# Kernel tuning notes

Measured on AMD Instinct MI355X. Metric: run time of the kernel, lower is better.

The kernel has to match this reference:

```python
import jax, jax.numpy as jnp
import numpy as np

N = 50000      # nodes
E = 800000     # edges (before self loops)
H = 2          # attention heads
CH = 64        # per-head hidden channels
IN = 128       # input features
OUT = 64       # output channels
EPS = 1e-5     # batchnorm eps
SLOPE = 0.2    # LeakyReLU negative slope


def _gat_conv(x, src, dst, W, a_src, a_dst, b, concat):
    # x: [N, Fin]; W: [Fin, H*C]; a_src/a_dst: [H, C]
    n = x.shape[0]
    h = (x @ W).reshape(n, H, -1)                       # [N, H, C]
    al_s = (h * a_src).sum(-1)                          # [N, H]
    al_d = (h * a_dst).sum(-1)                          # [N, H]
    e = al_s[src] + al_d[dst]                           # [E, H]
    e = jnp.where(e > 0, e, SLOPE * e)                  # LeakyReLU
    # softmax over edges grouped by destination node
    m = jax.ops.segment_max(e, dst, num_segments=n)
    ex = jnp.exp(e - m[dst])
    den = jax.ops.segment_sum(ex, dst, num_segments=n)
    alpha = ex / (den[dst] + 1e-16)                     # [E, H]
    out = jax.ops.segment_sum(h[src] * alpha[:, :, None], dst, num_segments=n)
    out = out.reshape(n, -1) if concat else out.mean(axis=1)
    return out + b


def _batchnorm(x, g, be):
    mu = x.mean(axis=0)
    var = x.var(axis=0)  # biased, as torch BN uses in training
    return (x - mu) * jax.lax.rsqrt(var + EPS) * g + be


def setup_inputs() -> dict:
    key = jax.random.key(0)
    ks = jax.random.split(key, 18)
    s = 0.1
    inp = {
        "x": jax.random.normal(ks[0], (N, IN), jnp.float32),
        "edge_index": jax.random.randint(ks[1], (2, E), 0, N, jnp.int64),
        # layer 0: IN -> H*CH (concat)
        "W0": jax.random.normal(ks[2], (IN, H * CH), jnp.float32) * s,
        "a_src0": jax.random.normal(ks[3], (H, CH), jnp.float32) * s,
        "a_dst0": jax.random.normal(ks[4], (H, CH), jnp.float32) * s,
        "b0": jnp.zeros((H * CH,), jnp.float32),
        "g0": jnp.ones((H * CH,), jnp.float32),
        "be0": jnp.zeros((H * CH,), jnp.float32),
        # layer 1: H*CH -> H*CH (concat)
        "W1": jax.random.normal(ks[5], (H * CH, H * CH), jnp.float32) * s,
        "a_src1": jax.random.normal(ks[6], (H, CH), jnp.float32) * s,
        "a_dst1": jax.random.normal(ks[7], (H, CH), jnp.float32) * s,
        "b1": jnp.zeros((H * CH,), jnp.float32),
        "g1": jnp.ones((H * CH,), jnp.float32),
        "be1": jnp.zeros((H * CH,), jnp.float32),
        # layer 2: H*CH -> OUT, concat=False (mean over heads)
        "W2": jax.random.normal(ks[8], (H * CH, H * OUT), jnp.float32) * s,
        "a_src2": jax.random.normal(ks[9], (H, OUT), jnp.float32) * s,
        "a_dst2": jax.random.normal(ks[10], (H, OUT), jnp.float32) * s,
        "b2": jnp.zeros((OUT,), jnp.float32),
    }
    return inp


def reference(x, edge_index, W0, a_src0, a_dst0, b0, g0, be0,
              W1, a_src1, a_dst1, b1, g1, be1,
              W2, a_src2, a_dst2, b2):
    # add self loops (PyG GATConv default)
    loop = jnp.arange(N, dtype=edge_index.dtype)
    src = jnp.concatenate([edge_index[0], loop])
    dst = jnp.concatenate([edge_index[1], loop])

    h = _gat_conv(x, src, dst, W0, a_src0, a_dst0, b0, concat=True)
    h = jax.nn.relu(_batchnorm(h, g0, be0))
    # dropout: eval mode (identity)
    h = _gat_conv(h, src, dst, W1, a_src1, a_dst1, b1, concat=True)
    h = jax.nn.relu(_batchnorm(h, g1, be1))
    out = _gat_conv(h, src, dst, W2, a_src2, a_dst2, b2, concat=False)
    return out
```

## Files before the change

### kernel.cpp

```cpp
#include <hip/hip_runtime.h>


#define N_NODES 50000
#define N_EDGES 800000
#define ET (N_EDGES + N_NODES)
#define FDIM 128
#define SLOPE 0.2f
#define BN_EPS 1e-5f
#define SCAN_NB 196
#define LOG2E 1.44269504088896340736f
#define WSTRIDE 18432

typedef __attribute__((ext_vector_type(8))) short bf16x8;
typedef __attribute__((ext_vector_type(4))) float f32x4;
typedef __attribute__((ext_vector_type(8))) unsigned short u16x8;

__device__ __forceinline__ unsigned short f2bf(float f) {
  unsigned u = __float_as_uint(f);
  u = u + 0x7fffu + ((u >> 16) & 1u);
  return (unsigned short)(u >> 16);
}
__device__ __forceinline__ float bflo(unsigned p) { return __uint_as_float(p << 16); }
__device__ __forceinline__ float bfhi(unsigned p) { return __uint_as_float(p & 0xffff0000u); }


__global__ __launch_bounds__(256) void hist_rank(const int* __restrict__ dst,
                                                 int* __restrict__ counts,
                                                 int* __restrict__ rank) {
  int i = blockIdx.x * 256 + threadIdx.x;
  if (i >= ET) return;
  int d = (i < N_EDGES) ? dst[i] : i - N_EDGES;
  rank[i] = atomicAdd(&counts[d], 1);
}

__global__ __launch_bounds__(256) void scan_blk(const int* __restrict__ counts,
                                                int* __restrict__ rowptr,
                                                int* __restrict__ partials) {
  int i = blockIdx.x * 256 + threadIdx.x;
  int lane = threadIdx.x & 63, wv = threadIdx.x >> 6;
  int c = (i < N_NODES) ? counts[i] : 0;
  int v = c;
#pragma unroll
  for (int off = 1; off < 64; off <<= 1) {
    int u = __shfl_up(v, off);
    if (lane >= off) v += u;
  }
  __shared__ int wsum[4];
  if (lane == 63) wsum[wv] = v;
  __syncthreads();
  int add = 0;
  for (int w = 0; w < wv; ++w) add += wsum[w];
  if (i < N_NODES) rowptr[i] = v - c + add;
  if (threadIdx.x == 255) partials[blockIdx.x] = add + v;
}

__global__ __launch_bounds__(256) void scan_fin(int* __restrict__ rowptr,
                                                const int* __restrict__ partials) {
  __shared__ int sh[256];
  int t = threadIdx.x;
  sh[t] = (t < (int)blockIdx.x && t < SCAN_NB) ? partials[t] : 0;
  __syncthreads();
#pragma unroll
  for (int off = 128; off > 0; off >>= 1) {
    if (t < off) sh[t] += sh[t + off];
    __syncthreads();
  }
  int base = sh[0];
  int i = blockIdx.x * 256 + t;
  if (i < N_NODES) rowptr[i] += base;
  if (i == 0) rowptr[N_NODES] = ET;
}

__global__ __launch_bounds__(256) void scatter_pos(const int* __restrict__ src,
                                                   const int* __restrict__ dst,
                                                   const int* __restrict__ rowptr,
                                                   const int* __restrict__ rank,
                                                   int* __restrict__ csr_src) {
  int i = blockIdx.x * 256 + threadIdx.x;
  if (i >= ET) return;
  int d, s;
  if (i < N_EDGES) { d = dst[i]; s = src[i]; } else { d = s = i - N_EDGES; }
  csr_src[rowptr[d] + rank[i]] = s;
}

__global__ __launch_bounds__(256) void repack_w(const float* __restrict__ W0,
                                                const float* __restrict__ W1,
                                                const float* __restrict__ W2,
                                                const float* __restrict__ as0,
                                                const float* __restrict__ as1,
                                                const float* __restrict__ as2,
                                                const float* __restrict__ ad0,
                                                const float* __restrict__ ad1,
                                                const float* __restrict__ ad2,
                                                unsigned short* __restrict__ Wr) {
  int i = blockIdx.x * 256 + threadIdx.x;
  if (i >= 3 * WSTRIDE) return;
  int L = i / WSTRIDE, rem = i % WSTRIDE;
  int t  = rem >> 11;
  int ks = (rem >> 9) & 3;
  int ln = (rem >> 3) & 63;
  int j  = rem & 7;
  int k  = ks * 32 + (ln >> 4) * 8 + j;
  const float* W = (L == 0) ? W0 : ((L == 1) ? W1 : W2);
  float val;
  if (t < 8) {
    int col = t * 16 + (ln & 15);
    val = W[k * 128 + col];
  } else {
    int cl = ln & 15;
    if (cl < 4) {
      int head = cl & 1;
      const float* a = (cl < 2) ? ((L == 0) ? as0 : (L == 1) ? as1 : as2)
                                : ((L == 0) ? ad0 : (L == 1) ? ad1 : ad2);
      float s = 0.f;
      const float* wrow = W + k * 128 + head * 64;
      const float* ah = a + head * 64;
#pragma unroll 8
      for (int c = 0; c < 64; ++c) s = fmaf(wrow[c], ah[c], s);
      val = s * LOG2E;
    } else {
      val = 0.f;
    }
  }
  Wr[i] = f2bf(val);
}

__global__ __launch_bounds__(128) void bn_fin(const float* __restrict__ part,
                                              const float* __restrict__ g,
                                              const float* __restrict__ be,
                                              float* __restrict__ lsbuf) {
  int t = threadIdx.x;
  float s = 0.f, q = 0.f;
#pragma unroll
  for (int k = 0; k < 32; ++k) {
    s += part[k * 256 + t];
    q += part[k * 256 + 128 + t];
  }
  float mu  = s * (1.f / N_NODES);
  float var = q * (1.f / N_NODES) - mu * mu;
  float sc  = rsqrtf(var + BN_EPS) * g[t];
  lsbuf[t]       = sc;
  lsbuf[128 + t] = be[t] - mu * sc;
}

__global__ __launch_bounds__(256) void gemm_mfma(const void* __restrict__ Xin,
                                                 const unsigned short* __restrict__ WrL,
                                                 const float* __restrict__ lsbuf,
                                                 unsigned short* __restrict__ Hbf,
                                                 float* __restrict__ als,
                                                 float* __restrict__ ald,
                                                 int inBF) {
  __shared__ unsigned short lds[4][16][128];
  __shared__ float ls_scale[128], ls_shift[128];
  int lane = threadIdx.x & 63;
  int wv   = threadIdx.x >> 6;

  if (inBF) {
    int t = threadIdx.x;
    if (t < 128) {
      ls_scale[t] = lsbuf[t];
      ls_shift[t] = lsbuf[128 + t];
    }
    __syncthreads();
  }

  int row0 = blockIdx.x * 64 + wv * 16;
  int gidx = lane & 15;
  int quad = lane >> 4;
  int rA   = row0 + gidx;
  int rAc  = rA < N_NODES ? rA : N_NODES - 1;
  int koff = quad * 8;

  f32x4 acc[9] = {};
#pragma unroll
  for (int ks = 0; ks < 4; ++ks) {
    int cb = ks * 32 + koff;
    float xv[8];
    if (inBF) {
      const uint4* xr = (const uint4*)((const unsigned*)Xin + (size_t)rAc * 64 + (cb >> 1));
      uint4 xa = *xr;
      xv[0] = bflo(xa.x); xv[1] = bfhi(xa.x);
      xv[2] = bflo(xa.y); xv[3] = bfhi(xa.y);
      xv[4] = bflo(xa.z); xv[5] = bfhi(xa.z);
      xv[6] = bflo(xa.w); xv[7] = bfhi(xa.w);
    } else {
      const float4* xr = (const float4*)((const float*)Xin + (size_t)rAc * FDIM + cb);
      float4 xa = xr[0], xb = xr[1];
      xv[0] = xa.x; xv[1] = xa.y; xv[2] = xa.z; xv[3] = xa.w;
      xv[4] = xb.x; xv[5] = xb.y; xv[6] = xb.z; xv[7] = xb.w;
    }
    bf16x8 afrag;
    if (inBF) {
#pragma unroll
      for (int j = 0; j < 8; ++j) {
        int c = cb + j;
        float v = fmaf(xv[j], ls_scale[c], ls_shift[c]);
        v = v > 0.f ? v : 0.f;
        afrag[j] = (short)f2bf(v);
      }
    } else {
#pragma unroll
      for (int j = 0; j < 8; ++j) afrag[j] = (short)f2bf(xv[j]);
    }
#pragma unroll
    for (int t = 0; t < 9; ++t) {
      bf16x8 bfrag = *(const bf16x8*)(WrL + ((size_t)((t * 4 + ks) * 64 + lane)) * 8);
      acc[t] = __builtin_amdgcn_mfma_f32_16x16x32_bf16(afrag, bfrag, acc[t], 0, 0, 0);
    }
  }

  if (gidx < 4) {
    float* dp = (gidx < 2) ? als : ald;
    int hd = gidx & 1;
#pragma unroll
    for (int r = 0; r < 4; ++r) {
      int row = row0 + quad * 4 + r;
      if (row < N_NODES) dp[row * 2 + hd] = acc[8][r];
    }
  }

#pragma unroll
  for (int t = 0; t < 8; ++t)
#pragma unroll
    for (int r = 0; r < 4; ++r)
      lds[wv][quad * 4 + r][t * 16 + gidx] = f2bf(acc[t][r]);
  __syncthreads();
#pragma unroll
  for (int it = 0; it < 4; ++it) {
    int rloc = it * 4 + quad;
    int row = row0 + rloc;
    if (row < N_NODES)
      *(u16x8*)(Hbf + (size_t)row * FDIM + gidx * 8) = *(u16x8*)&lds[wv][rloc][gidx * 8];
  }
}

__global__ __launch_bounds__(256) void fused_agg(const int* __restrict__ rowptr,
                                                 const int* __restrict__ csr_src,
                                                 const unsigned* __restrict__ H2,
                                                 const float* __restrict__ als,
                                                 const float* __restrict__ ald,
                                                 unsigned* __restrict__ Abf,
                                                 float* __restrict__ out,
                                                 const float* __restrict__ b2,
                                                 float* __restrict__ part,
                                                 int mode) {
  int lane = threadIdx.x & 63;
  bool hi = lane >= 32;
  int n = __builtin_amdgcn_readfirstlane((blockIdx.x * 256 + threadIdx.x) >> 6);
  int beg = rowptr[n], end = rowptr[n + 1];
  float2 adv = ((const float2*)ald)[n];
  float advh = hi ? adv.y : adv.x;

  int b0 = end - 8; if (b0 > beg) b0 = beg; if (b0 < 0) b0 = 0;
  int delta = beg - b0;
  int sa[8]; float2 aa[8]; unsigned ha[8];
#pragma unroll
  for (int i = 0; i < 8; ++i) sa[i] = csr_src[b0 + i];
#pragma unroll
  for (int i = 0; i < 8; ++i) {
    aa[i] = ((const float2*)als)[sa[i]];
    ha[i] = H2[(size_t)sa[i] * 64 + lane];
  }

  float l = 0.f, ox = 0.f, oy = 0.f;

#define STEP(i) { \
    float v_ = (hi ? aa[i].y : aa[i].x) + advh; \
    v_ = fmaxf(v_, SLOPE * v_); \
    float e_ = exp2f(v_); \
    l += e_; \
    ox = fmaf(e_, bflo(ha[i]), ox); \
    oy = fmaf(e_, bfhi(ha[i]), oy); }

  int j = beg;
  for (; j + 8 <= end; j += 8) {
    int pp = j + 8; if (pp > end - 8) pp = end - 8;
    int sn[8]; float2 an[8]; unsigned hn[8];
#pragma unroll
    for (int i = 0; i < 8; ++i) sn[i] = csr_src[pp + i];
#pragma unroll
    for (int i = 0; i < 8; ++i) {
      an[i] = ((const float2*)als)[sn[i]];
      hn[i] = H2[(size_t)sn[i] * 64 + lane];
    }
    STEP(0); STEP(1); STEP(2); STEP(3); STEP(4); STEP(5); STEP(6); STEP(7);
    delta = j + 8 - pp;
#pragma unroll
    for (int i = 0; i < 8; ++i) { aa[i] = an[i]; ha[i] = hn[i]; }
  }
  int rem = end - j;
  int hik = delta + rem;
  if (0 >= delta && 0 < hik) STEP(0);
  if (1 >= delta && 1 < hik) STEP(1);
  if (2 >= delta && 2 < hik) STEP(2);
  if (3 >= delta && 3 < hik) STEP(3);
  if (4 >= delta && 4 < hik) STEP(4);
  if (5 >= delta && 5 < hik) STEP(5);
  if (6 >= delta && 6 < hik) STEP(6);
  if (7 >= delta && 7 < hik) STEP(7);
#undef STEP

  float inv = 1.f / (l + 1e-16f);
  ox *= inv; oy *= inv;

  if (mode == 0) {
    unsigned pack = ((unsigned)f2bf(oy) << 16) | (unsigned)f2bf(ox);
    Abf[(size_t)n * 64 + lane] = pack;
    __shared__ float sh[4][4][64];
    int wv = threadIdx.x >> 6;
    sh[wv][0][lane] = ox;
    sh[wv][1][lane] = oy;
    sh[wv][2][lane] = ox * ox;
    sh[wv][3][lane] = oy * oy;
    __syncthreads();
    if (threadIdx.x < 64) {
      int t = threadIdx.x;
      float a0 = 0.f, a1 = 0.f, a2 = 0.f, a3 = 0.f;
#pragma unroll
      for (int w = 0; w < 4; ++w) {
        a0 += sh[w][0][t]; a1 += sh[w][1][t];
        a2 += sh[w][2][t]; a3 += sh[w][3][t];
      }
      float* slot = part + (blockIdx.x & 31) * 256;
      atomicAdd(&slot[2 * t],           a0);
      atomicAdd(&slot[2 * t + 1],       a1);
      atomicAdd(&slot[128 + 2 * t],     a2);
      atomicAdd(&slot[128 + 2 * t + 1], a3);
    }
  } else {
    float px = __shfl_xor(ox, 32);
    float py = __shfl_xor(oy, 32);
    if (lane < 32) {
      int c = lane * 2;
      float2 outv = {0.5f * (ox + px) + b2[c], 0.5f * (oy + py) + b2[c + 1]};
      *(float2*)(out + (size_t)n * 64 + c) = outv;
    }
  }
}

extern "C" void kernel_launch(void* const* d_in, const int* in_sizes, int n_in,
                              void* d_out, int out_size, void* d_ws, size_t ws_size,
                              hipStream_t stream) {
  const float* x  = (const float*)d_in[0];
  const int*   ei = (const int*)d_in[1];
  const int* src = ei;
  const int* dst = ei + N_EDGES;

  const float* W[3]    = {(const float*)d_in[2],  (const float*)d_in[8],  (const float*)d_in[14]};
  const float* asrc[3] = {(const float*)d_in[3],  (const float*)d_in[9],  (const float*)d_in[15]};
  const float* adst[3] = {(const float*)d_in[4],  (const float*)d_in[10], (const float*)d_in[16]};
  const float* g[2]    = {(const float*)d_in[6],  (const float*)d_in[12]};
  const float* be[2]   = {(const float*)d_in[7],  (const float*)d_in[13]};
  const float* b2      = (const float*)d_in[17];

  int*   counts   = (int*)d_ws;
  int*   rowptr   = counts + 50048;
  int*   partials = rowptr + 50048;
  int*   rank     = partials + 256;
  int*   csr_src  = rank + 850048;
  float* part     = (float*)(csr_src + 850048);
  float* lsbuf    = part + 8192;
  float* als      = lsbuf + 256;
  float* ald      = als + 100096;
  unsigned short* Wr  = (unsigned short*)(ald + 100096);
  unsigned short* Hbf = Wr + 3 * WSTRIDE + 128;
  unsigned* Abf   = (unsigned*)(Hbf + (size_t)N_NODES * FDIM);

  hipMemsetAsync(counts, 0, (size_t)N_NODES * sizeof(int), stream);
  hist_rank<<<(ET + 255) / 256, 256, 0, stream>>>(dst, counts, rank);
  scan_blk<<<SCAN_NB, 256, 0, stream>>>(counts, rowptr, partials);
  scan_fin<<<SCAN_NB, 256, 0, stream>>>(rowptr, partials);
  scatter_pos<<<(ET + 255) / 256, 256, 0, stream>>>(src, dst, rowptr, rank, csr_src);
  repack_w<<<(3 * WSTRIDE + 255) / 256, 256, 0, stream>>>(
      W[0], W[1], W[2], asrc[0], asrc[1], asrc[2], adst[0], adst[1], adst[2], Wr);

  const int gemm_grid = (N_NODES + 63) / 64;
  const int agg_grid  = N_NODES * 64 / 256;

  for (int L = 0; L < 3; ++L) {
    const void* fin = (L == 0) ? (const void*)x : (const void*)Abf;
    int inBF = (L > 0);
    gemm_mfma<<<gemm_grid, 256, 0, stream>>>(fin, Wr + (size_t)L * WSTRIDE, lsbuf,
                                             Hbf, als, ald, inBF);
    if (L < 2)
      hipMemsetAsync(part, 0, 8192 * sizeof(float), stream);
    fused_agg<<<agg_grid, 256, 0, stream>>>(rowptr, csr_src, (const unsigned*)Hbf,
                                            als, ald, Abf, (float*)d_out, b2, part,
                                            (L == 2) ? 2 : 0);
    if (L < 2)
      bn_fin<<<1, 128, 0, stream>>>(part, g[L], be[L], lsbuf);
  }
}
```

Measured before the change: 339.8 us.

## Split edge aggregation into lane-parallel score phase and LDS-staged gather phase

The per-node aggregation is restructured so that each 32-lane half-wave first computes attention scores for up to 32 edges in parallel (one edge per lane), staging the source index and exp weight in LDS with double buffering. A second phase then walks the staged entries, gathering bf16 features and accumulating weighted sums, and the denominator is reduced with a lane shuffle. This removes the redundant per-lane score and exp computation the old serial 8-edge unrolled loop did on every lane. In exchange it adds LDS traffic, an extra shuffle reduction, and for low-degree nodes a chunk that is mostly idle lanes.

Result: no change. 342.1 us (+0.7%).

```diff
diff --git a/kernel.cpp b/kernel.cpp
--- a/kernel.cpp
+++ b/kernel.cpp
@@ -244,70 +244,64 @@
                                                  const float* __restrict__ b2,
                                                  float* __restrict__ part,
                                                  int mode) {
+  __shared__ float2 se[4][2][32][2];
   int lane = threadIdx.x & 63;
-  bool hi = lane >= 32;
+  int li   = lane & 31;
+  int hd   = lane >> 5;
+  int wv   = threadIdx.x >> 6;
   int n = __builtin_amdgcn_readfirstlane((blockIdx.x * 256 + threadIdx.x) >> 6);
   int beg = rowptr[n], end = rowptr[n + 1];
-  float2 adv = ((const float2*)ald)[n];
-  float advh = hi ? adv.y : adv.x;
-
-  int b0 = end - 8; if (b0 > beg) b0 = beg; if (b0 < 0) b0 = 0;
-  int delta = beg - b0;
-  int sa[8]; float2 aa[8]; unsigned ha[8];
-#pragma unroll
-  for (int i = 0; i < 8; ++i) sa[i] = csr_src[b0 + i];
-#pragma unroll
-  for (int i = 0; i < 8; ++i) {
-    aa[i] = ((const float2*)als)[sa[i]];
-    ha[i] = H2[(size_t)sa[i] * 64 + lane];
-  }
-
-  float l = 0.f, ox = 0.f, oy = 0.f;
-
-#define STEP(i) { \
-    float v_ = (hi ? aa[i].y : aa[i].x) + advh; \
+  float advh = ald[n * 2 + hd];
+
+  float lpart = 0.f, ox = 0.f, oy = 0.f;
+
+#define PHASE1(c_, buf_) { \
+    int cnt_ = end - (c_); if (cnt_ > 32) cnt_ = 32; \
+    int idx_ = (c_) + (li < cnt_ ? li : cnt_ - 1); \
+    int s_ = csr_src[idx_]; \
+    float v_ = als[s_ * 2 + hd] + advh; \
     v_ = fmaxf(v_, SLOPE * v_); \
-    float e_ = exp2f(v_); \
-    l += e_; \
-    ox = fmaf(e_, bflo(ha[i]), ox); \
-    oy = fmaf(e_, bfhi(ha[i]), oy); }
-
-  int j = beg;
-  for (; j + 8 <= end; j += 8) {
-    int pp = j + 8; if (pp > end - 8) pp = end - 8;
-    int sn[8]; float2 an[8]; unsigned hn[8];
-#pragma unroll
-    for (int i = 0; i < 8; ++i) sn[i] = csr_src[pp + i];
-#pragma unroll
-    for (int i = 0; i < 8; ++i) {
-      an[i] = ((const float2*)als)[sn[i]];
-      hn[i] = H2[(size_t)sn[i] * 64 + lane];
-    }
-    STEP(0); STEP(1); STEP(2); STEP(3); STEP(4); STEP(5); STEP(6); STEP(7);
-    delta = j + 8 - pp;
-#pragma unroll
-    for (int i = 0; i < 8; ++i) { aa[i] = an[i]; ha[i] = hn[i]; }
-  }
-  int rem = end - j;
-  int hik = delta + rem;
-  if (0 >= delta && 0 < hik) STEP(0);
-  if (1 >= delta && 1 < hik) STEP(1);
-  if (2 >= delta && 2 < hik) STEP(2);
-  if (3 >= delta && 3 < hik) STEP(3);
-  if (4 >= delta && 4 < hik) STEP(4);
-  if (5 >= delta && 5 < hik) STEP(5);
-  if (6 >= delta && 6 < hik) STEP(6);
-  if (7 >= delta && 7 < hik) STEP(7);
-#undef STEP
-
-  float inv = 1.f / (l + 1e-16f);
+    float e_ = (li < cnt_) ? exp2f(v_) : 0.f; \
+    lpart += e_; \
+    se[wv][buf_][li][hd] = make_float2(__int_as_float(s_), e_); }
+
+#define P2STEP(p_) { \
+    unsigned q_ = H2[(size_t)__float_as_uint((p_).x) * 64 + lane]; \
+    ox = fmaf((p_).y, bflo(q_), ox); \
+    oy = fmaf((p_).y, bfhi(q_), oy); }
+
+  PHASE1(beg, 0);
+  int buf = 0;
+  for (int c = beg; c < end; c += 32) {
+    if (c + 32 < end) PHASE1(c + 32, buf ^ 1);
+    int cnt = end - c; if (cnt > 32) cnt = 32;
+    int j = 0;
+    for (; j + 4 <= cnt; j += 4) {
+      float2 p0 = se[wv][buf][j + 0][hd];
+      float2 p1 = se[wv][buf][j + 1][hd];
+      float2 p2 = se[wv][buf][j + 2][hd];
+      float2 p3 = se[wv][buf][j + 3][hd];
+      P2STEP(p0); P2STEP(p1); P2STEP(p2); P2STEP(p3);
+    }
+    for (; j < cnt; ++j) {
+      float2 p = se[wv][buf][j][hd];
+      P2STEP(p);
+    }
+    buf ^= 1;
+  }
+#undef PHASE1
+#undef P2STEP
+
+#pragma unroll
+  for (int off = 1; off < 32; off <<= 1) lpart += __shfl_xor(lpart, off);
+
+  float inv = 1.f / (lpart + 1e-16f);
   ox *= inv; oy *= inv;
 
   if (mode == 0) {
     unsigned pack = ((unsigned)f2bf(oy) << 16) | (unsigned)f2bf(ox);
     Abf[(size_t)n * 64 + lane] = pack;
     __shared__ float sh[4][4][64];
-    int wv = threadIdx.x >> 6;
     sh[wv][0][lane] = ox;
     sh[wv][1][lane] = oy;
     sh[wv][2][lane] = ox * ox;
```

## Stage GEMM input tile through LDS and partition CSR scatter by node range

Applied to the files above, without the earlier changes.

The GEMM kernel now loads each 64-row input tile cooperatively with coalesced row-wise reads, applies the BN scale/shift/ReLU and bf16 conversion once per element, and stores it into a padded LDS tile from which MFMA A-fragments are read. It then reuses the same LDS buffer for the output transpose. The CSR scatter is restructured so each block handles one of 8 destination-node ranges over a chunk of edges. This is meant to improve write locality, at the cost of every block re-reading dst for edges it then skips.

Result: slower. 353.2 us (+3.9%).

```diff
diff --git a/kernel.cpp b/kernel.cpp
--- a/kernel.cpp
+++ b/kernel.cpp
@@ -10,6 +10,10 @@
 #define SCAN_NB 196
 #define LOG2E 1.44269504088896340736f
 #define WSTRIDE 18432
+#define NRANGE 8
+#define RNODES (N_NODES / NRANGE)
+#define SCAT_SUB 96
+#define SCAT_CH ((ET + SCAT_SUB - 1) / SCAT_SUB)
 
 typedef __attribute__((ext_vector_type(8))) short bf16x8;
 typedef __attribute__((ext_vector_type(4))) float f32x4;
@@ -19,6 +23,9 @@
   unsigned u = __float_as_uint(f);
   u = u + 0x7fffu + ((u >> 16) & 1u);
   return (unsigned short)(u >> 16);
+}
+__device__ __forceinline__ unsigned packbf(float lo, float hi) {
+  return ((unsigned)f2bf(hi) << 16) | (unsigned)f2bf(lo);
 }
 __device__ __forceinline__ float bflo(unsigned p) { return __uint_as_float(p << 16); }
 __device__ __forceinline__ float bfhi(unsigned p) { return __uint_as_float(p & 0xffff0000u); }
@@ -76,11 +83,18 @@
                                                    const int* __restrict__ rowptr,
                                                    const int* __restrict__ rank,
                                                    int* __restrict__ csr_src) {
-  int i = blockIdx.x * 256 + threadIdx.x;
-  if (i >= ET) return;
-  int d, s;
-  if (i < N_EDGES) { d = dst[i]; s = src[i]; } else { d = s = i - N_EDGES; }
-  csr_src[rowptr[d] + rank[i]] = s;
+  int r = blockIdx.x & (NRANGE - 1);
+  int s = blockIdx.x >> 3;
+  int lo = r * RNODES, hi = lo + RNODES;
+  int e0 = s * SCAT_CH;
+  int e1 = e0 + SCAT_CH; if (e1 > ET) e1 = ET;
+  for (int i = e0 + threadIdx.x; i < e1; i += 256) {
+    int d = (i < N_EDGES) ? dst[i] : i - N_EDGES;
+    if (d >= lo && d < hi) {
+      int sv = (i < N_EDGES) ? src[i] : d;
+      csr_src[rowptr[d] + rank[i]] = sv;
+    }
+  }
 }
 
 __global__ __launch_bounds__(256) void repack_w(const float* __restrict__ W0,
@@ -150,58 +164,63 @@
                                                  float* __restrict__ als,
                                                  float* __restrict__ ald,
                                                  int inBF) {
-  __shared__ unsigned short lds[4][16][128];
+  __shared__ unsigned short xt[64][136];
   __shared__ float ls_scale[128], ls_shift[128];
-  int lane = threadIdx.x & 63;
-  int wv   = threadIdx.x >> 6;
+  int tid = threadIdx.x;
+  int row0 = blockIdx.x * 64;
 
   if (inBF) {
-    int t = threadIdx.x;
-    if (t < 128) {
-      ls_scale[t] = lsbuf[t];
-      ls_shift[t] = lsbuf[128 + t];
+    if (tid < 128) {
+      ls_scale[tid] = lsbuf[tid];
+      ls_shift[tid] = lsbuf[128 + tid];
     }
     __syncthreads();
   }
 
-  int row0 = blockIdx.x * 64 + wv * 16;
+  {
+    int r = tid >> 2;
+    int q = tid & 3;
+    int row = row0 + r;
+    int rc = row < N_NODES ? row : N_NODES - 1;
+    unsigned* xr = (unsigned*)&xt[0][0] + r * 68;
+    if (inBF) {
+      const uint4* p = (const uint4*)((const unsigned*)Xin + (size_t)rc * 64 + q * 16);
+#pragma unroll
+      for (int b = 0; b < 4; ++b) {
+        uint4 v = p[b];
+        unsigned wbase = q * 16 + b * 4;
+        unsigned wv[4] = {v.x, v.y, v.z, v.w};
+#pragma unroll
+        for (int k = 0; k < 4; ++k) {
+          int c = (wbase + k) * 2;
+          float f0 = fmaf(bflo(wv[k]), ls_scale[c],     ls_shift[c]);
+          float f1 = fmaf(bfhi(wv[k]), ls_scale[c + 1], ls_shift[c + 1]);
+          f0 = f0 > 0.f ? f0 : 0.f;
+          f1 = f1 > 0.f ? f1 : 0.f;
+          xr[wbase + k] = packbf(f0, f1);
+        }
+      }
+    } else {
+      const float4* p = (const float4*)((const float*)Xin + (size_t)rc * FDIM + q * 32);
+#pragma unroll
+      for (int b = 0; b < 8; ++b) {
+        float4 v = p[b];
+        int w = q * 16 + b * 2;
+        xr[w]     = packbf(v.x, v.y);
+        xr[w + 1] = packbf(v.z, v.w);
+      }
+    }
+  }
+  __syncthreads();
+
+  int lane = tid & 63;
+  int wv   = tid >> 6;
   int gidx = lane & 15;
   int quad = lane >> 4;
-  int rA   = row0 + gidx;
-  int rAc  = rA < N_NODES ? rA : N_NODES - 1;
-  int koff = quad * 8;
-
   f32x4 acc[9] = {};
 #pragma unroll
   for (int ks = 0; ks < 4; ++ks) {
-    int cb = ks * 32 + koff;
-    float xv[8];
-    if (inBF) {
-      const uint4* xr = (const uint4*)((const unsigned*)Xin + (size_t)rAc * 64 + (cb >> 1));
-      uint4 xa = *xr;
-      xv[0] = bflo(xa.x); xv[1] = bfhi(xa.x);
-      xv[2] = bflo(xa.y); xv[3] = bfhi(xa.y);
-      xv[4] = bflo(xa.z); xv[5] = bfhi(xa.z);
-      xv[6] = bflo(xa.w); xv[7] = bfhi(xa.w);
-    } else {
-      const float4* xr = (const float4*)((const float*)Xin + (size_t)rAc * FDIM + cb);
-      float4 xa = xr[0], xb = xr[1];
-      xv[0] = xa.x; xv[1] = xa.y; xv[2] = xa.z; xv[3] = xa.w;
-      xv[4] = xb.x; xv[5] = xb.y; xv[6] = xb.z; xv[7] = xb.w;
-    }
-    bf16x8 afrag;
-    if (inBF) {
-#pragma unroll
-      for (int j = 0; j < 8; ++j) {
-        int c = cb + j;
-        float v = fmaf(xv[j], ls_scale[c], ls_shift[c]);
-        v = v > 0.f ? v : 0.f;
-        afrag[j] = (short)f2bf(v);
-      }
-    } else {
-#pragma unroll
-      for (int j = 0; j < 8; ++j) afrag[j] = (short)f2bf(xv[j]);
-    }
+    bf16x8 afrag = *(const bf16x8*)&xt[wv * 16 + gidx][ks * 32 + quad * 8];
 #pragma unroll
     for (int t = 0; t < 9; ++t) {
       bf16x8 bfrag = *(const bf16x8*)(WrL + ((size_t)((t * 4 + ks) * 64 + lane)) * 8);
@@ -209,28 +228,32 @@
     }
   }
 
+  int wrow0 = row0 + wv * 16;
   if (gidx < 4) {
     float* dp = (gidx < 2) ? als : ald;
     int hd = gidx & 1;
 #pragma unroll
     for (int r = 0; r < 4; ++r) {
-      int row = row0 + quad * 4 + r;
+      int row = wrow0 + quad * 4 + r;
       if (row < N_NODES) dp[row * 2 + hd] = acc[8][r];
     }
   }
 
+  __syncthreads();
+  unsigned short* tr = &xt[0][0];
 #pragma unroll
   for (int t = 0; t < 8; ++t)
 #pragma unroll
     for (int r = 0; r < 4; ++r)
-      lds[wv][quad * 4 + r][t * 16 + gidx] = f2bf(acc[t][r]);
+      tr[wv * 2048 + (quad * 4 + r) * 128 + t * 16 + gidx] = f2bf(acc[t][r]);
   __syncthreads();
 #pragma unroll
   for (int it = 0; it < 4; ++it) {
     int rloc = it * 4 + quad;
-    int row = row0 + rloc;
+    int row = wrow0 + rloc;
     if (row < N_NODES)
-      *(u16x8*)(Hbf + (size_t)row * FDIM + gidx * 8) = *(u16x8*)&lds[wv][rloc][gidx * 8];
+      *(u16x8*)(Hbf + (size_t)row * FDIM + gidx * 8) =
+          *(u16x8*)&tr[wv * 2048 + rloc * 128 + gidx * 8];
   }
 }
 
@@ -304,8 +327,7 @@
   ox *= inv; oy *= inv;
 
   if (mode == 0) {
-    unsigned pack = ((unsigned)f2bf(oy) << 16) | (unsigned)f2bf(ox);
-    Abf[(size_t)n * 64 + lane] = pack;
+    Abf[(size_t)n * 64 + lane] = packbf(ox, oy);
     __shared__ float sh[4][4][64];
     int wv = threadIdx.x >> 6;
     sh[wv][0][lane] = ox;
@@ -370,7 +392,7 @@
   hist_rank<<<(ET + 255) / 256, 256, 0, stream>>>(dst, counts, rank);
   scan_blk<<<SCAN_NB, 256, 0, stream>>>(counts, rowptr, partials);
   scan_fin<<<SCAN_NB, 256, 0, stream>>>(rowptr, partials);
-  scatter_pos<<<(ET + 255) / 256, 256, 0, stream>>>(src, dst, rowptr, rank, csr_src);
+  scatter_pos<<<NRANGE * SCAT_SUB, 256, 0, stream>>>(src, dst, rowptr, rank, csr_src);
   repack_w<<<(3 * WSTRIDE + 255) / 256, 256, 0, stream>>>(
       W[0], W[1], W[2], asrc[0], asrc[1], asrc[2], adst[0], adst[1], adst[2], Wr);
 
```

## Sort nodes by in-degree for aggregation wave scheduling; zero BN partials in bn_fin

Applied to the files above, without the earlier changes.

Adds a counting sort of nodes by in-degree, in descending order (histogram, scan, scatter), and has each aggregation wave pick its node from the resulting order. Heavy nodes then start first and waves within a block see similar amounts of work, which aims to reduce load imbalance and tail effects. The per-layer memset of the BN partial buffer is dropped: bn_fin now clears the partials after reading them, and one memset runs up front. The cost is three extra small setup kernels, plus an extra indirection and less locality in the node order for output writes.

Result: slower. 625.6 us (+84.1%).

```diff
diff --git a/kernel.cpp b/kernel.cpp
--- a/kernel.cpp
+++ b/kernel.cpp
@@ -20,6 +20,9 @@
   u = u + 0x7fffu + ((u >> 16) & 1u);
   return (unsigned short)(u >> 16);
 }
+__device__ __forceinline__ unsigned packbf(float lo, float hi) {
+  return ((unsigned)f2bf(hi) << 16) | (unsigned)f2bf(lo);
+}
 __device__ __forceinline__ float bflo(unsigned p) { return __uint_as_float(p << 16); }
 __device__ __forceinline__ float bfhi(unsigned p) { return __uint_as_float(p & 0xffff0000u); }
 
@@ -81,6 +84,35 @@
   int d, s;
   if (i < N_EDGES) { d = dst[i]; s = src[i]; } else { d = s = i - N_EDGES; }
   csr_src[rowptr[d] + rank[i]] = s;
+}
+
+__global__ __launch_bounds__(256) void deg_hist(const int* __restrict__ counts,
+                                                int* __restrict__ dh) {
+  int i = blockIdx.x * 256 + threadIdx.x;
+  if (i >= N_NODES) return;
+  int d = counts[i]; if (d > 255) d = 255;
+  atomicAdd(&dh[d], 1);
+}
+
+__global__ __launch_bounds__(256) void deg_scan(const int* __restrict__ dh,
+                                                int* __restrict__ dfill) {
+  __shared__ int sh[256];
+  int t = threadIdx.x;
+  sh[t] = dh[t];
+  __syncthreads();
+  int off = 0;
+  for (int d = t + 1; d < 256; ++d) off += sh[d];
+  dfill[t] = off;
+}
+
+__global__ __launch_bounds__(256) void deg_scat(const int* __restrict__ counts,
+                                                int* __restrict__ dfill,
+                                                int* __restrict__ order) {
+  int i = blockIdx.x * 256 + threadIdx.x;
+  if (i >= N_NODES) return;
+  int d = counts[i]; if (d > 255) d = 255;
+  int pos = atomicAdd(&dfill[d], 1);
+  order[pos] = i;
 }
 
 __global__ __launch_bounds__(256) void repack_w(const float* __restrict__ W0,
@@ -125,7 +157,7 @@
   Wr[i] = f2bf(val);
 }
 
-__global__ __launch_bounds__(128) void bn_fin(const float* __restrict__ part,
+__global__ __launch_bounds__(128) void bn_fin(float* __restrict__ part,
                                               const float* __restrict__ g,
                                               const float* __restrict__ be,
                                               float* __restrict__ lsbuf) {
@@ -135,6 +167,8 @@
   for (int k = 0; k < 32; ++k) {
     s += part[k * 256 + t];
     q += part[k * 256 + 128 + t];
+    part[k * 256 + t] = 0.f;
+    part[k * 256 + 128 + t] = 0.f;
   }
   float mu  = s * (1.f / N_NODES);
   float var = q * (1.f / N_NODES) - mu * mu;
@@ -234,7 +268,8 @@
   }
 }
 
-__global__ __launch_bounds__(256) void fused_agg(const int* __restrict__ rowptr,
+__global__ __launch_bounds__(256) void fused_agg(const int* __restrict__ order,
+                                                 const int* __restrict__ rowptr,
                                                  const int* __restrict__ csr_src,
                                                  const unsigned* __restrict__ H2,
                                                  const float* __restrict__ als,
@@ -246,7 +281,8 @@
                                                  int mode) {
   int lane = threadIdx.x & 63;
   bool hi = lane >= 32;
-  int n = __builtin_amdgcn_readfirstlane((blockIdx.x * 256 + threadIdx.x) >> 6);
+  int wid = (blockIdx.x * 256 + threadIdx.x) >> 6;
+  int n = __builtin_amdgcn_readfirstlane(order[wid]);
   int beg = rowptr[n], end = rowptr[n + 1];
   float2 adv = ((const float2*)ald)[n];
   float advh = hi ? adv.y : adv.x;
@@ -304,8 +340,7 @@
   ox *= inv; oy *= inv;
 
   if (mode == 0) {
-    unsigned pack = ((unsigned)f2bf(oy) << 16) | (unsigned)f2bf(ox);
-    Abf[(size_t)n * 64 + lane] = pack;
+    Abf[(size_t)n * 64 + lane] = packbf(ox, oy);
     __shared__ float sh[4][4][64];
     int wv = threadIdx.x >> 6;
     sh[wv][0][lane] = ox;
@@ -358,7 +393,10 @@
   int*   partials = rowptr + 50048;
   int*   rank     = partials + 256;
   int*   csr_src  = rank + 850048;
-  float* part     = (float*)(csr_src + 850048);
+  int*   order    = csr_src + 850048;
+  int*   dh       = order + 50048;
+  int*   dfill    = dh + 256;
+  float* part     = (float*)(dfill + 256);
   float* lsbuf    = part + 8192;
   float* als      = lsbuf + 256;
   float* ald      = als + 100096;
@@ -367,10 +405,15 @@
   unsigned* Abf   = (unsigned*)(Hbf + (size_t)N_NODES * FDIM);
 
   hipMemsetAsync(counts, 0, (size_t)N_NODES * sizeof(int), stream);
+  hipMemsetAsync(dh, 0, 256 * sizeof(int), stream);
+  hipMemsetAsync(part, 0, 8192 * sizeof(float), stream);
   hist_rank<<<(ET + 255) / 256, 256, 0, stream>>>(dst, counts, rank);
   scan_blk<<<SCAN_NB, 256, 0, stream>>>(counts, rowptr, partials);
   scan_fin<<<SCAN_NB, 256, 0, stream>>>(rowptr, partials);
   scatter_pos<<<(ET + 255) / 256, 256, 0, stream>>>(src, dst, rowptr, rank, csr_src);
+  deg_hist<<<SCAN_NB, 256, 0, stream>>>(counts, dh);
+  deg_scan<<<1, 256, 0, stream>>>(dh, dfill);
+  deg_scat<<<SCAN_NB, 256, 0, stream>>>(counts, dfill, order);
   repack_w<<<(3 * WSTRIDE + 255) / 256, 256, 0, stream>>>(
       W[0], W[1], W[2], asrc[0], asrc[1], asrc[2], adst[0], adst[1], adst[2], Wr);
 
@@ -382,9 +425,8 @@
     int inBF = (L > 0);
     gemm_mfma<<<gemm_grid, 256, 0, stream>>>(fin, Wr + (size_t)L * WSTRIDE, lsbuf,
                                              Hbf, als, ald, inBF);
-    if (L < 2)
-      hipMemsetAsync(part, 0, 8192 * sizeof(float), stream);
-    fused_agg<<<agg_grid, 256, 0, stream>>>(rowptr, csr_src, (const unsigned*)Hbf,
+    fused_agg<<<agg_grid, 256, 0, stream>>>(order, rowptr, csr_src,
+                                            (const unsigned*)Hbf,
                                             als, ald, Abf, (float*)d_out, b2, part,
                                             (L == 2) ? 2 : 0);
     if (L < 2)
```
